# Kernel tuning notes

Measured on AMD Instinct MI355X. Metric: run time of the kernel, lower is better.

Reference implementation:

```python
import jax, jax.numpy as jnp
import numpy as np

D_MODEL = 1024

def setup_inputs() -> dict:
    key = jax.random.key(0)
    ks = jax.random.split(key, 7)
    x = jax.random.normal(ks[0], (4, 4096, D_MODEL), dtype=jnp.float32)
    s = 1.0 / np.sqrt(D_MODEL)
    Wq = jax.random.uniform(ks[1], (D_MODEL, D_MODEL), jnp.float32, -s, s)
    bq = jax.random.uniform(ks[2], (D_MODEL,), jnp.float32, -s, s)
    Wk = jax.random.uniform(ks[3], (D_MODEL, D_MODEL), jnp.float32, -s, s)
    bk = jax.random.uniform(ks[4], (D_MODEL,), jnp.float32, -s, s)
    Wv = jax.random.uniform(ks[5], (D_MODEL, D_MODEL), jnp.float32, -s, s)
    bv = jax.random.uniform(ks[6], (D_MODEL,), jnp.float32, -s, s)
    return {"x": x, "Wq": Wq, "bq": bq, "Wk": Wk, "bk": bk, "Wv": Wv, "bv": bv}

def reference(x, Wq, bq, Wk, bk, Wv, bv):
    # Q, K, V: [b, s, d]
    Q = jnp.einsum('bsd,ed->bse', x, Wq) + bq
    K = jnp.einsum('bsd,ed->bse', x, Wk) + bk
    V = jnp.einsum('bsd,ed->bse', x, Wv) + bv
    scale = 1.0 / jnp.sqrt(jnp.asarray(D_MODEL, dtype=x.dtype))
    scores = jnp.einsum('bqd,bkd->bqk', Q, K) * scale  # [b, s, s]
    attn = jax.nn.softmax(scores, axis=-1)
    return jnp.einsum('bqk,bkd->bqd', attn, V)
```

## Files before the change

### kernel.cpp

```cpp
#include <hip/hip_runtime.h>
#include <stdint.h>
#include <stddef.h>

#define DM 1024
#define SEQ 4096
#define NB 4
#define NTOK (NB*SEQ)

typedef __attribute__((ext_vector_type(8))) short s16x8;
typedef __attribute__((ext_vector_type(4))) float f32x4;

__device__ __forceinline__ unsigned short f2bf(float f) {
  unsigned int u = __float_as_uint(f);
  u += 0x7FFFu + ((u >> 16) & 1u);
  return (unsigned short)(u >> 16);
}
__device__ __forceinline__ float bf2f(unsigned short u) {
  return __uint_as_float((unsigned int)u << 16);
}

__device__ __forceinline__ f32x4 mfma16(s16x8 a, s16x8 b, f32x4 c) {
  return __builtin_amdgcn_mfma_f32_16x16x32_bf16(a, b, c, 0, 0, 0);
}

__device__ __forceinline__ void gload16(const void* g, void* l) {
  __builtin_amdgcn_global_load_lds((const __attribute__((address_space(1))) unsigned int*)g,
                                   (__attribute__((address_space(3))) unsigned int*)l, 16, 0, 0);
}

__device__ __forceinline__ void xcd_swz(int gx, int gy, int& x, int& y, int& z) {
  int nwg = gx * gy * gridDim.z;
  int bid = blockIdx.x + gx * (blockIdx.y + gy * blockIdx.z);
  int cpx = nwg >> 3;
  int wg = (bid & 7) * cpx + (bid >> 3);
  x = wg % gx; int t = wg / gx; y = t % gy; z = t / gy;
}

__global__ void k_conv(const float* __restrict__ s, unsigned short* __restrict__ d, int n8) {
  int i = blockIdx.x * blockDim.x + threadIdx.x;
  int st = gridDim.x * blockDim.x;
  for (; i < n8; i += st) {
    const f32x4* sp = (const f32x4*)s + (size_t)i * 2;
    f32x4 a = sp[0], b = sp[1];
    s16x8 o;
    o[0] = (short)f2bf(a[0]); o[1] = (short)f2bf(a[1]);
    o[2] = (short)f2bf(a[2]); o[3] = (short)f2bf(a[3]);
    o[4] = (short)f2bf(b[0]); o[5] = (short)f2bf(b[1]);
    o[6] = (short)f2bf(b[2]); o[7] = (short)f2bf(b[3]);
    *((s16x8*)d + i) = o;
  }
}

template<int KD, int BK, int EPI>
__device__ __forceinline__ void gemm_core(
    unsigned short (*lds)[2][128 * BK],
    const unsigned short* __restrict__ A, const unsigned short* __restrict__ B,
    void* __restrict__ outp, int ldc, const float* __restrict__ aux, float scale,
    int mbase, int nbase)
{
  constexpr int NT     = KD / BK;
  constexpr int SLOTS  = BK / 8;
  constexpr int SMASK  = SLOTS - 1;
  constexpr int PASSES = 128 * SLOTS / 256;

  const int tid = threadIdx.x, lane = tid & 63, wid = tid >> 6;
  const int wr = wid >> 1, wc = wid & 1;
  const int l15 = lane & 15, lg = lane >> 4;

  f32x4 acc[4][4];
  #pragma unroll
  for (int m = 0; m < 4; m++)
    #pragma unroll
    for (int n = 0; n < 4; n++) { acc[m][n][0]=0.f; acc[m][n][1]=0.f; acc[m][n][2]=0.f; acc[m][n][3]=0.f; }

  auto rswz = [](int row) -> int { return (BK == 64) ? (row & 7) : ((row >> 1) & 3); };

  auto stage = [&](int buf, int kt) {
    const int kb_ = kt * BK;
    #pragma unroll
    for (int p = 0; p < PASSES; p++) {
      int s = p * 256 + tid;
      int row = s / SLOTS, sl = (s & SMASK) ^ rswz(row);
      gload16(A + (size_t)(mbase + row) * KD + kb_ + sl * 8, &lds[buf][0][s * 8]);
    }
    #pragma unroll
    for (int p = 0; p < PASSES; p++) {
      int s = p * 256 + tid;
      int row = s / SLOTS, sl = (s & SMASK) ^ rswz(row);
      gload16(B + (size_t)(nbase + row) * KD + kb_ + sl * 8, &lds[buf][1][s * 8]);
    }
  };

  auto compute = [&](int buf) {
    #pragma unroll
    for (int k2 = 0; k2 < BK / 32; k2++) {
      s16x8 af[4], bf[4];
      #pragma unroll
      for (int m = 0; m < 4; m++) {
        int row = wr * 64 + m * 16 + l15;
        int sl = (k2 * 4 + lg) ^ rswz(row);
        af[m] = *(const s16x8*)(&lds[buf][0][0] + row * BK + sl * 8);
      }
      #pragma unroll
      for (int n = 0; n < 4; n++) {
        int row = wc * 64 + n * 16 + l15;
        int sl = (k2 * 4 + lg) ^ rswz(row);
        bf[n] = *(const s16x8*)(&lds[buf][1][0] + row * BK + sl * 8);
      }
      #pragma unroll
      for (int m = 0; m < 4; m++)
        #pragma unroll
        for (int n = 0; n < 4; n++)
          acc[m][n] = mfma16(af[m], bf[n], acc[m][n]);
    }
  };

  stage(0, 0);
  __syncthreads();
  for (int kt = 0; kt < NT; kt++) {
    int cur = kt & 1;
    if (kt < NT - 1) stage(cur ^ 1, kt + 1);
    compute(cur);
    __syncthreads();
  }

  #pragma unroll
  for (int n = 0; n < 4; n++) {
    int col = nbase + wc * 64 + n * 16 + l15;
    float cb = (EPI == 0) ? aux[col] : 0.f;
    #pragma unroll
    for (int m = 0; m < 4; m++) {
      #pragma unroll
      for (int r = 0; r < 4; r++) {
        int row = mbase + wr * 64 + m * 16 + lg * 4 + r;
        float v = acc[m][n][r];
        if (EPI == 0) {
          ((unsigned short*)outp)[(size_t)row * ldc + col] = f2bf(v + cb);
        } else if (EPI == 1) {
          ((unsigned short*)outp)[(size_t)row * ldc + col] = f2bf(__expf(v * scale));
        } else if (EPI == 3) {
          ((unsigned short*)outp)[(size_t)row * ldc + col] = f2bf(v + aux[row]);
        } else {
          ((float*)outp)[(size_t)row * ldc + col] = v * aux[row];
        }
      }
    }
  }
}

__global__ __launch_bounds__(256, 4) void k_qkv(
    const unsigned short* __restrict__ xb, const unsigned short* __restrict__ wb,
    const float* __restrict__ b0, const float* __restrict__ b1, const float* __restrict__ bv,
    unsigned short* __restrict__ qo, unsigned short* __restrict__ ko, unsigned short* __restrict__ vt)
{
  __shared__ unsigned short lds[2][2][128 * 32];
  int x, y, z;
  xcd_swz(8, 128, x, y, z);
  if (z < 2) {
    gemm_core<DM, 32, 0>(lds, xb, wb + (size_t)z * DM * DM,
                         z ? ko : qo, DM, z ? b1 : b0, 0.f,
                         y * 128, x * 128);
  } else {
    int batch = y >> 5, tokb = (y & 31) * 128;
    gemm_core<DM, 32, 3>(lds, wb + (size_t)2 * DM * DM, xb + (size_t)batch * SEQ * DM,
                         vt + (size_t)batch * DM * SEQ, SEQ, bv, 0.f,
                         x * 128, tokb);
  }
}

__global__ __launch_bounds__(256, 4) void k_sgemm(
    const unsigned short* __restrict__ qb, const unsigned short* __restrict__ kb,
    unsigned short* __restrict__ s0, unsigned short* __restrict__ s1,
    unsigned short* __restrict__ s2, unsigned short* __restrict__ s3, int bb)
{
  __shared__ unsigned short lds[2][2][128 * 32];
  int x, y, z;
  xcd_swz(32, 32, x, y, z);
  unsigned short* sc = (z == 0) ? s0 : (z == 1) ? s1 : (z == 2) ? s2 : s3;
  gemm_core<DM, 32, 1>(lds, qb + (size_t)(bb + z) * SEQ * DM, kb + (size_t)(bb + z) * SEQ * DM,
                       sc, SEQ, nullptr, 0.03125f,
                       y * 128, x * 128);
}

__global__ __launch_bounds__(256) void k_rowsum(
    const unsigned short* __restrict__ s0, const unsigned short* __restrict__ s1,
    const unsigned short* __restrict__ s2, const unsigned short* __restrict__ s3,
    float* __restrict__ linv, int bb) {
  const int z = blockIdx.z;
  const unsigned short* sc = (z == 0) ? s0 : (z == 1) ? s1 : (z == 2) ? s2 : s3;
  const int row = blockIdx.x * 4 + (threadIdx.x >> 6);
  const int lane = threadIdx.x & 63;
  const unsigned short* rp = sc + (size_t)row * SEQ + lane * 8;
  float s = 0.f;
  #pragma unroll
  for (int j = 0; j < 8; j++) {
    s16x8 v = *(const s16x8*)(rp + (size_t)j * 512);
    #pragma unroll
    for (int t = 0; t < 8; t++) s += bf2f((unsigned short)v[t]);
  }
  s += __shfl_xor(s, 1);  s += __shfl_xor(s, 2);  s += __shfl_xor(s, 4);
  s += __shfl_xor(s, 8);  s += __shfl_xor(s, 16); s += __shfl_xor(s, 32);
  if (lane == 0) linv[(size_t)(bb + z) * SEQ + row] = 1.f / s;
}

template<int BK>
__global__ __launch_bounds__(256, (BK == 32) ? 4 : 2) void k_pv(
    const unsigned short* __restrict__ s0, const unsigned short* __restrict__ s1,
    const unsigned short* __restrict__ s2, const unsigned short* __restrict__ s3,
    const unsigned short* __restrict__ vt, const float* __restrict__ linv,
    float* __restrict__ out, int bb)
{
  __shared__ unsigned short lds[2][2][128 * BK];
  int x, y, z;
  xcd_swz(8, 32, x, y, z);
  const unsigned short* sc = (z == 0) ? s0 : (z == 1) ? s1 : (z == 2) ? s2 : s3;
  gemm_core<SEQ, BK, 4>(lds, sc, vt + (size_t)(bb + z) * DM * SEQ,
                        out + (size_t)(bb + z) * SEQ * DM, DM,
                        linv + (size_t)(bb + z) * SEQ, 1.f,
                        y * 128, x * 128);
}

extern "C" void kernel_launch(void* const* d_in, const int* in_sizes, int n_in,
                              void* d_out, int out_size, void* d_ws, size_t ws_size,
                              hipStream_t stream) {
  const float* x  = (const float*)d_in[0];
  const float* Wq = (const float*)d_in[1];
  const float* bq = (const float*)d_in[2];
  const float* Wk = (const float*)d_in[3];
  const float* bk = (const float*)d_in[4];
  const float* Wv = (const float*)d_in[5];
  const float* bv = (const float*)d_in[6];
  float* out = (float*)d_out;
  char* ws = (char*)d_ws;

  unsigned short* xb  = (unsigned short*)(ws);
  unsigned short* wb  = (unsigned short*)(ws + 33554432);
  unsigned short* qb  = (unsigned short*)(ws + 39845888);
  unsigned short* kb  = (unsigned short*)(ws + 73400320);
  unsigned short* sc1 = (unsigned short*)(ws + 106954752);
  unsigned short* vt  = (unsigned short*)(ws + 140509184);
  float* linv         = (float*)(ws + 174063616);
  unsigned short* sc0 = xb;
  unsigned short* sc2 = (unsigned short*)(ws + 174129152);
  unsigned short* sc3 = (unsigned short*)(ws + 207683584);
  const bool big = ws_size >= 241238016ull;

  k_conv<<<4096, 256, 0, stream>>>(x, xb, NTOK * DM / 8);
  k_conv<<<512, 256, 0, stream>>>(Wq, wb, DM * DM / 8);
  k_conv<<<512, 256, 0, stream>>>(Wk, wb + DM * DM, DM * DM / 8);
  k_conv<<<512, 256, 0, stream>>>(Wv, wb + 2 * DM * DM, DM * DM / 8);

  k_qkv<<<dim3(8, 128, 3), 256, 0, stream>>>(xb, wb, bq, bk, bv, qb, kb, vt);

  if (big) {
    k_sgemm<<<dim3(32, 32, 4), 256, 0, stream>>>(qb, kb, sc0, sc1, sc2, sc3, 0);
    k_rowsum<<<dim3(1024, 1, 4), 256, 0, stream>>>(sc0, sc1, sc2, sc3, linv, 0);
    k_pv<32><<<dim3(8, 32, 4), 256, 0, stream>>>(sc0, sc1, sc2, sc3, vt, linv, out, 0);
  } else {
    for (int bb = 0; bb < NB; bb += 2) {
      k_sgemm<<<dim3(32, 32, 2), 256, 0, stream>>>(qb, kb, sc0, sc1, sc0, sc1, bb);
      k_rowsum<<<dim3(1024, 1, 2), 256, 0, stream>>>(sc0, sc1, sc0, sc1, linv, bb);
      k_pv<64><<<dim3(8, 32, 2), 256, 0, stream>>>(sc0, sc1, sc0, sc1, vt, linv, out, bb);
    }
  }
}
```

Measured before the change: 508.5 us.

## Fuse softmax row-sum into score GEMM epilogue and merge conversion kernels

Removes the separate row-sum kernel by having the score GEMM epilogue accumulate per-row exp sums through wave shuffles and float atomicAdd into a zeroed buffer. The PV kernel now computes the reciprocals itself from that buffer. The four fp32-to-bf16 conversion launches become a single kernel that also zeroes the sum buffer, and launch-bounds occupancy hints go from 4 to 5. This avoids rereading the whole bf16 score matrix and cuts launch overhead, at the cost of atomic traffic and more register pressure under the higher occupancy hint.

```diff
diff --git a/kernel.cpp b/kernel.cpp
--- a/kernel.cpp
+++ b/kernel.cpp
@@ -36,18 +36,31 @@
   x = wg % gx; int t = wg / gx; y = t % gy; z = t / gy;
 }
 
-__global__ void k_conv(const float* __restrict__ s, unsigned short* __restrict__ d, int n8) {
-  int i = blockIdx.x * blockDim.x + threadIdx.x;
+__global__ void k_conv4(const float* __restrict__ x, const float* __restrict__ wq,
+                        const float* __restrict__ wk, const float* __restrict__ wv,
+                        unsigned short* __restrict__ xb, unsigned short* __restrict__ wb,
+                        float* __restrict__ lsum) {
+  const int n0 = NTOK * DM / 8;
+  const int n1 = DM * DM / 8;
+  int i0 = blockIdx.x * blockDim.x + threadIdx.x;
   int st = gridDim.x * blockDim.x;
-  for (; i < n8; i += st) {
-    const f32x4* sp = (const f32x4*)s + (size_t)i * 2;
+  for (int i = i0; i < NTOK; i += st) lsum[i] = 0.f;
+  for (int i = i0; i < n0 + 3 * n1; i += st) {
+    const float* s; unsigned short* d; int k;
+    if (i < n0) { s = x; d = xb; k = i; }
+    else {
+      int j = i - n0; int seg = j >> 17; k = j & (n1 - 1);
+      s = (seg == 0) ? wq : (seg == 1) ? wk : wv;
+      d = wb + (size_t)seg * DM * DM;
+    }
+    const f32x4* sp = (const f32x4*)s + (size_t)k * 2;
     f32x4 a = sp[0], b = sp[1];
     s16x8 o;
     o[0] = (short)f2bf(a[0]); o[1] = (short)f2bf(a[1]);
     o[2] = (short)f2bf(a[2]); o[3] = (short)f2bf(a[3]);
     o[4] = (short)f2bf(b[0]); o[5] = (short)f2bf(b[1]);
     o[6] = (short)f2bf(b[2]); o[7] = (short)f2bf(b[3]);
-    *((s16x8*)d + i) = o;
+    *((s16x8*)d + k) = o;
   }
 }
 
@@ -56,7 +69,7 @@
     unsigned short (*lds)[2][128 * BK],
     const unsigned short* __restrict__ A, const unsigned short* __restrict__ B,
     void* __restrict__ outp, int ldc, const float* __restrict__ aux, float scale,
-    int mbase, int nbase)
+    float* __restrict__ redu, int mbase, int nbase)
 {
   constexpr int NT     = KD / BK;
   constexpr int SLOTS  = BK / 8;
@@ -124,6 +137,18 @@
     __syncthreads();
   }
 
+  float linv_r[16];
+  if (EPI == 4) {
+    #pragma unroll
+    for (int i = 0; i < 16; i++)
+      linv_r[i] = 1.f / redu[mbase + wr * 64 + (i >> 2) * 16 + lg * 4 + (i & 3)];
+  }
+  float rowpart[16];
+  if (EPI == 1) {
+    #pragma unroll
+    for (int i = 0; i < 16; i++) rowpart[i] = 0.f;
+  }
+
   #pragma unroll
   for (int n = 0; n < 4; n++) {
     int col = nbase + wc * 64 + n * 16 + l15;
@@ -137,18 +162,31 @@
         if (EPI == 0) {
           ((unsigned short*)outp)[(size_t)row * ldc + col] = f2bf(v + cb);
         } else if (EPI == 1) {
-          ((unsigned short*)outp)[(size_t)row * ldc + col] = f2bf(__expf(v * scale));
+          float e = __expf(v * scale);
+          ((unsigned short*)outp)[(size_t)row * ldc + col] = f2bf(e);
+          rowpart[m * 4 + r] += e;
         } else if (EPI == 3) {
           ((unsigned short*)outp)[(size_t)row * ldc + col] = f2bf(v + aux[row]);
         } else {
-          ((float*)outp)[(size_t)row * ldc + col] = v * aux[row];
+          ((float*)outp)[(size_t)row * ldc + col] = v * linv_r[m * 4 + r];
         }
       }
     }
   }
-}
-
-__global__ __launch_bounds__(256, 4) void k_qkv(
+
+  if (EPI == 1) {
+    #pragma unroll
+    for (int i = 0; i < 16; i++) {
+      float rs = rowpart[i];
+      rs += __shfl_xor(rs, 1); rs += __shfl_xor(rs, 2);
+      rs += __shfl_xor(rs, 4); rs += __shfl_xor(rs, 8);
+      if (l15 == 0)
+        atomicAdd(&redu[mbase + wr * 64 + (i >> 2) * 16 + lg * 4 + (i & 3)], rs);
+    }
+  }
+}
+
+__global__ __launch_bounds__(256, 5) void k_qkv(
     const unsigned short* __restrict__ xb, const unsigned short* __restrict__ wb,
     const float* __restrict__ b0, const float* __restrict__ b1, const float* __restrict__ bv,
     unsigned short* __restrict__ qo, unsigned short* __restrict__ ko, unsigned short* __restrict__ vt)
@@ -158,56 +196,36 @@
   xcd_swz(8, 128, x, y, z);
   if (z < 2) {
     gemm_core<DM, 32, 0>(lds, xb, wb + (size_t)z * DM * DM,
-                         z ? ko : qo, DM, z ? b1 : b0, 0.f,
+                         z ? ko : qo, DM, z ? b1 : b0, 0.f, nullptr,
                          y * 128, x * 128);
   } else {
     int batch = y >> 5, tokb = (y & 31) * 128;
     gemm_core<DM, 32, 3>(lds, wb + (size_t)2 * DM * DM, xb + (size_t)batch * SEQ * DM,
-                         vt + (size_t)batch * DM * SEQ, SEQ, bv, 0.f,
+                         vt + (size_t)batch * DM * SEQ, SEQ, bv, 0.f, nullptr,
                          x * 128, tokb);
   }
 }
 
-__global__ __launch_bounds__(256, 4) void k_sgemm(
+__global__ __launch_bounds__(256, 5) void k_sgemm(
     const unsigned short* __restrict__ qb, const unsigned short* __restrict__ kb,
     unsigned short* __restrict__ s0, unsigned short* __restrict__ s1,
-    unsigned short* __restrict__ s2, unsigned short* __restrict__ s3, int bb)
+    unsigned short* __restrict__ s2, unsigned short* __restrict__ s3,
+    float* __restrict__ lsum, int bb)
 {
   __shared__ unsigned short lds[2][2][128 * 32];
   int x, y, z;
   xcd_swz(32, 32, x, y, z);
   unsigned short* sc = (z == 0) ? s0 : (z == 1) ? s1 : (z == 2) ? s2 : s3;
   gemm_core<DM, 32, 1>(lds, qb + (size_t)(bb + z) * SEQ * DM, kb + (size_t)(bb + z) * SEQ * DM,
-                       sc, SEQ, nullptr, 0.03125f,
+                       sc, SEQ, nullptr, 0.03125f, lsum + (size_t)(bb + z) * SEQ,
                        y * 128, x * 128);
 }
 
-__global__ __launch_bounds__(256) void k_rowsum(
+template<int BK>
+__global__ __launch_bounds__(256, (BK == 32) ? 5 : 2) void k_pv(
     const unsigned short* __restrict__ s0, const unsigned short* __restrict__ s1,
     const unsigned short* __restrict__ s2, const unsigned short* __restrict__ s3,
-    float* __restrict__ linv, int bb) {
-  const int z = blockIdx.z;
-  const unsigned short* sc = (z == 0) ? s0 : (z == 1) ? s1 : (z == 2) ? s2 : s3;
-  const int row = blockIdx.x * 4 + (threadIdx.x >> 6);
-  const int lane = threadIdx.x & 63;
-  const unsigned short* rp = sc + (size_t)row * SEQ + lane * 8;
-  float s = 0.f;
-  #pragma unroll
-  for (int j = 0; j < 8; j++) {
-    s16x8 v = *(const s16x8*)(rp + (size_t)j * 512);
-    #pragma unroll
-    for (int t = 0; t < 8; t++) s += bf2f((unsigned short)v[t]);
-  }
-  s += __shfl_xor(s, 1);  s += __shfl_xor(s, 2);  s += __shfl_xor(s, 4);
-  s += __shfl_xor(s, 8);  s += __shfl_xor(s, 16); s += __shfl_xor(s, 32);
-  if (lane == 0) linv[(size_t)(bb + z) * SEQ + row] = 1.f / s;
-}
-
-template<int BK>
-__global__ __launch_bounds__(256, (BK == 32) ? 4 : 2) void k_pv(
-    const unsigned short* __restrict__ s0, const unsigned short* __restrict__ s1,
-    const unsigned short* __restrict__ s2, const unsigned short* __restrict__ s3,
-    const unsigned short* __restrict__ vt, const float* __restrict__ linv,
+    const unsigned short* __restrict__ vt, float* __restrict__ lsum,
     float* __restrict__ out, int bb)
 {
   __shared__ unsigned short lds[2][2][128 * BK];
@@ -216,7 +234,7 @@
   const unsigned short* sc = (z == 0) ? s0 : (z == 1) ? s1 : (z == 2) ? s2 : s3;
   gemm_core<SEQ, BK, 4>(lds, sc, vt + (size_t)(bb + z) * DM * SEQ,
                         out + (size_t)(bb + z) * SEQ * DM, DM,
-                        linv + (size_t)(bb + z) * SEQ, 1.f,
+                        nullptr, 1.f, lsum + (size_t)(bb + z) * SEQ,
                         y * 128, x * 128);
 }
 
@@ -239,28 +257,22 @@
   unsigned short* kb  = (unsigned short*)(ws + 73400320);
   unsigned short* sc1 = (unsigned short*)(ws + 106954752);
   unsigned short* vt  = (unsigned short*)(ws + 140509184);
-  float* linv         = (float*)(ws + 174063616);
+  float* lsum         = (float*)(ws + 174063616);
   unsigned short* sc0 = xb;
   unsigned short* sc2 = (unsigned short*)(ws + 174129152);
   unsigned short* sc3 = (unsigned short*)(ws + 207683584);
   const bool big = ws_size >= 241238016ull;
 
-  k_conv<<<4096, 256, 0, stream>>>(x, xb, NTOK * DM / 8);
-  k_conv<<<512, 256, 0, stream>>>(Wq, wb, DM * DM / 8);
-  k_conv<<<512, 256, 0, stream>>>(Wk, wb + DM * DM, DM * DM / 8);
-  k_conv<<<512, 256, 0, stream>>>(Wv, wb + 2 * DM * DM, DM * DM / 8);
-
+  k_conv4<<<2048, 256, 0, stream>>>(x, Wq, Wk, Wv, xb, wb, lsum);
   k_qkv<<<dim3(8, 128, 3), 256, 0, stream>>>(xb, wb, bq, bk, bv, qb, kb, vt);
 
   if (big) {
-    k_sgemm<<<dim3(32, 32, 4), 256, 0, stream>>>(qb, kb, sc0, sc1, sc2, sc3, 0);
-    k_rowsum<<<dim3(1024, 1, 4), 256, 0, stream>>>(sc0, sc1, sc2, sc3, linv, 0);
-    k_pv<32><<<dim3(8, 32, 4), 256, 0, stream>>>(sc0, sc1, sc2, sc3, vt, linv, out, 0);
+    k_sgemm<<<dim3(32, 32, 4), 256, 0, stream>>>(qb, kb, sc0, sc1, sc2, sc3, lsum, 0);
+    k_pv<32><<<dim3(8, 32, 4), 256, 0, stream>>>(sc0, sc1, sc2, sc3, vt, lsum, out, 0);
   } else {
     for (int bb = 0; bb < NB; bb += 2) {
-      k_sgemm<<<dim3(32, 32, 2), 256, 0, stream>>>(qb, kb, sc0, sc1, sc0, sc1, bb);
-      k_rowsum<<<dim3(1024, 1, 2), 256, 0, stream>>>(sc0, sc1, sc0, sc1, linv, bb);
-      k_pv<64><<<dim3(8, 32, 2), 256, 0, stream>>>(sc0, sc1, sc0, sc1, vt, linv, out, bb);
-    }
-  }
-}
+      k_sgemm<<<dim3(32, 32, 2), 256, 0, stream>>>(qb, kb, sc0, sc1, sc0, sc1, lsum, bb);
+      k_pv<64><<<dim3(8, 32, 2), 256, 0, stream>>>(sc0, sc1, sc0, sc1, vt, lsum, out, bb);
+    }
+  }
+}
```

Measured after the change: 612.6 us. +20.5%, slower.
